# Performance work log

Hardware: AMD Instinct MI355X
Metric: run time of the kernel (lower is better)

The kernel has to match this reference:

```python
import jax, jax.numpy as jnp
import numpy as np

B, L, D, C, N, K = 4096, 4096, 1024, 64, 8192, 5
TEMP = 0.1
ALPHA = 2.0
EPS = 1e-12


def setup_inputs() -> dict:
    key = jax.random.key(0)
    ks = jax.random.split(key, 8)
    x = jax.random.normal(ks[0], (B, 1, L), jnp.float32)
    y = jax.random.randint(ks[1], (B,), 0, C)
    Wf = jax.random.normal(ks[2], (L, D), jnp.float32) * 0.02
    Wc = jax.random.normal(ks[3], (C, D), jnp.float32) * 0.02
    bc = jnp.zeros((C,), jnp.float32)
    supports_old = jax.random.normal(ks[4], (N, D), jnp.float32)
    scores_old = jax.nn.softmax(jax.random.normal(ks[5], (N, C), jnp.float32), axis=-1)
    labels_old = jax.nn.one_hot(jax.random.randint(ks[6], (N,), 0, C), C, dtype=jnp.float32)
    return dict(x=x, y=y, Wf=Wf, Wc=Wc, bc=bc, supports_old=supports_old,
                labels_old=labels_old, scores_old=scores_old)


def _l2n(v, axis):
    return v / jnp.maximum(jnp.linalg.norm(v, axis=axis, keepdims=True), EPS)


def _masked_mean(v, w):
    return jnp.sum(v * w) / jnp.maximum(jnp.sum(w), 1.0)


def _tta_loss(x, Wf, Wc, bc, supports_old, labels_old, scores_old):
    feats = x.reshape(B, L) @ Wf                      # [B, D] featurizer
    logits = feats @ Wc.T + bc                        # [B, C]
    probs = jax.nn.softmax(logits, -1)
    logp = jax.nn.log_softmax(logits, -1)
    prob = probs.max(-1)
    pred = jnp.argmax(logits, -1)
    # prediction-confidence filter
    y_certain = prob >= prob.mean()
    # input-energy entropy filter (scipy.stats.entropy over axis=2)
    px = x * x
    px = px / jnp.maximum(px.sum(2, keepdims=True), EPS)
    e = -(px * jnp.log(px + 1e-30)).sum(2).reshape(B)
    e_certain = e < e.mean()
    w_c = (e_certain & y_certain).astype(jnp.float32)  # certain mask as weights
    w_u = 1.0 - w_c
    yhat = jax.nn.one_hot(pred, C, dtype=jnp.float32)
    # --- memory bank concat + prototype build (no_grad in torch) ---
    sup_all = jnp.concatenate([supports_old, feats], 0)        # [N+B, D]
    lab_all = jnp.concatenate([labels_old, yhat], 0)           # [N+B, C]
    w_all = jnp.concatenate([jnp.ones((N,), jnp.float32), w_c], 0)
    lw = lab_all * w_all[:, None]
    protos = _l2n(sup_all, 1).T @ lw / jnp.maximum(lw.sum(0, keepdims=True), EPS)
    protos = jax.lax.stop_gradient(_l2n(protos, 0))            # [D, C]
    # --- loss1: Tsallis entropy - diversity on balanced probs ---
    m = jnp.sum(probs * w_c[:, None], 0) / jnp.maximum(w_c.sum(), 1.0)
    pb = probs / jnp.maximum(m, EPS)
    pb = pb / pb.sum(1, keepdims=True)
    tsallis = jnp.mean((1.0 - jnp.sum(pb ** ALPHA, 1)) / (ALPHA - 1.0))
    pm = pb.mean(0)
    div = -jnp.sum(pm * jnp.log(pm + EPS))
    loss1 = tsallis - div
    # --- loss2: PCL, prototype CE on certain samples (temp=1) ---
    lp = jax.nn.log_softmax(_l2n(feats, 1) @ protos, -1)       # [B, C]
    ce = -jnp.take_along_axis(lp, pred[:, None], 1)[:, 0]
    loss2 = _masked_mean(ce, w_c)
    # --- loss3: NCL, kNN soft targets from memory bank, uncertain rows ---
    scores_all = jax.lax.stop_gradient(jnp.concatenate([scores_old, probs], 0))
    sup_det = jax.lax.stop_gradient(sup_all)
    sim = _l2n(feats, 1) @ _l2n(sup_det, 1).T / TEMP           # [B, N+B]
    sim = jnp.where(w_all[None, :] > 0, sim, -jnp.inf)
    _, idx = jax.lax.top_k(sim, K)                             # [B, K]
    tgt = scores_all[idx].mean(1)                              # [B, C]
    ncl = -(tgt * logp).sum(1)
    loss3 = _masked_mean(ncl, w_u)
    return loss1 + loss2 + loss3


def reference(x, y, Wf, Wc, bc, supports_old, labels_old, scores_old):
    return _tta_loss(x, Wf, Wc, bc, supports_old, labels_old, scores_old)
```

## Files before the change

kernel.cpp:

```cpp
#include <hip/hip_runtime.h>
#include <math.h>

#define BBATCH 4096
#define LLEN   4096
#define DDIM   1024
#define CCLS   64
#define NSUP   8192
#define NTOT   12288
#define FEPS   1e-12f
#define KCHUNK 48
#define KCAND  (KCHUNK*6)

#define SC_SUMP  0
#define SC_SUME  1
#define SC_SUMWC 2
#define SC_TSAL  3
#define SC_L2NUM 4
#define SC_L3NUM 5

typedef _Float16 half4_t __attribute__((ext_vector_type(4)));
typedef _Float16 half8_t __attribute__((ext_vector_type(8)));
typedef float    f32x4   __attribute__((ext_vector_type(4)));
typedef float    f32x16  __attribute__((ext_vector_type(16)));

static const size_t OFF_FEATS  = 0;
static const size_t OFF_FEATP1 = OFF_FEATS  + (size_t)BBATCH*DDIM;
static const size_t OFF_WFTH   = OFF_FEATP1 + (size_t)BBATCH*DDIM;
static const size_t OFF_WFTL   = OFF_WFTH   + (size_t)DDIM*LLEN/2;
static const size_t OFF_PROBS  = OFF_WFTL   + (size_t)DDIM*LLEN/2;
static const size_t OFF_LOGP   = OFF_PROBS  + (size_t)BBATCH*CCLS;
static const size_t OFF_FNORM  = OFF_LOGP   + (size_t)BBATCH*CCLS;
static const size_t OFF_SNORM  = OFF_FNORM  + BBATCH;
static const size_t OFF_PMAX   = OFF_SNORM  + NSUP;
static const size_t OFF_EROW   = OFF_PMAX   + BBATCH;
static const size_t OFF_WC     = OFF_EROW   + BBATCH;
static const size_t OFF_PRED   = OFF_WC     + BBATCH;
static const size_t OFF_RB     = OFF_PRED   + BBATCH;
static const size_t OFF_SNM    = OFF_RB     + BBATCH;
static const size_t OFF_PROTOT = OFF_SNM    + NTOT;
static const size_t OFF_CVAL   = OFF_PROTOT + (size_t)CCLS*DDIM;
static const size_t OFF_CIDX   = OFF_CVAL   + (size_t)BBATCH*KCAND;
static const size_t OFF_ZERO   = OFF_CIDX   + (size_t)BBATCH*KCAND;
static const size_t OFF_MACC   = OFF_ZERO;
static const size_t OFF_PMACC  = OFF_MACC   + CCLS;
static const size_t OFF_COLS   = OFF_PMACC  + CCLS;
static const size_t OFF_SCAL   = OFF_COLS   + CCLS;
static const size_t OFF_PROTUN = OFF_SCAL   + 32;
static const size_t OFF_ZEND   = OFF_PROTUN + (size_t)DDIM*CCLS;
static const size_t OFF_HT     = OFF_ZEND;
static const size_t WS_END     = OFF_HT + (size_t)32*NTOT*32/2;

__device__ __forceinline__ float waveSum(float v){
  #pragma unroll
  for (int o = 32; o > 0; o >>= 1) v += __shfl_xor(v, o);
  return v;
}
__device__ __forceinline__ float waveMax(float v){
  #pragma unroll
  for (int o = 32; o > 0; o >>= 1) v = fmaxf(v, __shfl_xor(v, o));
  return v;
}
__device__ __forceinline__ float blockSum256(float v, float* sh4){
  v = waveSum(v);
  if ((threadIdx.x & 63) == 0) sh4[threadIdx.x >> 6] = v;
  __syncthreads();
  float r = sh4[0] + sh4[1] + sh4[2] + sh4[3];
  __syncthreads();
  return r;
}
__device__ __forceinline__ void top6_insert(float* v, int* ix, float s, int si){
  bool c0=s>v[0],c1=s>v[1],c2=s>v[2],c3=s>v[3],c4=s>v[4],c5=s>v[5];
  v[5]=c5?(c4?v[4]:s):v[5]; ix[5]=c5?(c4?ix[4]:si):ix[5];
  v[4]=c4?(c3?v[3]:s):v[4]; ix[4]=c4?(c3?ix[3]:si):ix[4];
  v[3]=c3?(c2?v[2]:s):v[3]; ix[3]=c3?(c2?ix[2]:si):ix[3];
  v[2]=c2?(c1?v[1]:s):v[2]; ix[2]=c2?(c1?ix[1]:si):ix[2];
  v[1]=c1?(c0?v[0]:s):v[1]; ix[1]=c1?(c0?ix[0]:si):ix[1];
  v[0]=c0?s:v[0];           ix[0]=c0?si:ix[0];
}
__device__ __forceinline__ void split4(const float4 v, half4_t* h, half4_t* l){
  half4_t hh, ll;
  hh[0] = (_Float16)v.x; hh[1] = (_Float16)v.y; hh[2] = (_Float16)v.z; hh[3] = (_Float16)v.w;
  ll[0] = (_Float16)(v.x - (float)hh[0]);
  ll[1] = (_Float16)(v.y - (float)hh[1]);
  ll[2] = (_Float16)(v.z - (float)hh[2]);
  ll[3] = (_Float16)(v.w - (float)hh[3]);
  *h = hh; *l = ll;
}
__device__ __forceinline__ void split8(const float4 a, const float4 b,
                                       half8_t* h, half8_t* l){
  half8_t hh, ll;
  hh[0]=(_Float16)a.x; hh[1]=(_Float16)a.y; hh[2]=(_Float16)a.z; hh[3]=(_Float16)a.w;
  hh[4]=(_Float16)b.x; hh[5]=(_Float16)b.y; hh[6]=(_Float16)b.z; hh[7]=(_Float16)b.w;
  ll[0]=(_Float16)(a.x-(float)hh[0]); ll[1]=(_Float16)(a.y-(float)hh[1]);
  ll[2]=(_Float16)(a.z-(float)hh[2]); ll[3]=(_Float16)(a.w-(float)hh[3]);
  ll[4]=(_Float16)(b.x-(float)hh[4]); ll[5]=(_Float16)(b.y-(float)hh[5]);
  ll[6]=(_Float16)(b.z-(float)hh[6]); ll[7]=(_Float16)(b.w-(float)hh[7]);
  *h = hh; *l = ll;
}
__device__ __forceinline__ size_t ht_off(int row, int d){
  int kt = d >> 5;
  int slot = ((d >> 3) & 3) ^ ((row >> 3) & 3);
  return (size_t)kt * (NTOT*32) + (size_t)row * 32 + slot*8 + (d & 7);
}

__global__ __launch_bounds__(256)
void k_entropy(const float* __restrict__ x, float* __restrict__ e_row,
               float* __restrict__ scal){
  __shared__ __align__(16) float lx[LLEN];
  __shared__ float sh4[4];
  int row = blockIdx.x, t = threadIdx.x;
  const float4* xr = (const float4*)(x + (size_t)row * LLEN);
  float s = 0.f;
  #pragma unroll
  for (int i = 0; i < 4; ++i){
    float4 v = xr[t + 256*i];
    ((float4*)lx)[t + 256*i] = v;
    s += v.x*v.x + v.y*v.y + v.z*v.z + v.w*v.w;
  }
  s = blockSum256(s, sh4);
  float inv = 1.0f / fmaxf(s, FEPS);
  float ent = 0.f;
  #pragma unroll
  for (int i = 0; i < 4; ++i){
    float4 v = ((float4*)lx)[t + 256*i];
    float p;
    p = v.x*v.x*inv; ent -= p * logf(p + 1e-30f);
    p = v.y*v.y*inv; ent -= p * logf(p + 1e-30f);
    p = v.z*v.z*inv; ent -= p * logf(p + 1e-30f);
    p = v.w*v.w*inv; ent -= p * logf(p + 1e-30f);
  }
  ent = blockSum256(ent, sh4);
  if (t == 0){ e_row[row] = ent; atomicAdd(&scal[SC_SUME], ent); }
}

__global__ __launch_bounds__(256)
void k_wft(const float* __restrict__ Wf, unsigned short* __restrict__ WftH,
           unsigned short* __restrict__ WftL){
  __shared__ __align__(16) float ld[64*68];
  int t = threadIdx.x;
  int d0 = blockIdx.x * 64;
  int l0 = blockIdx.y * 64;
  #pragma unroll
  for (int i = 0; i < 4; ++i){
    int flat = t + 256*i;
    int l = flat >> 4, d4 = (flat & 15) * 4;
    *(float4*)&ld[l*68 + d4] = *(const float4*)(Wf + (size_t)(l0+l)*DDIM + d0 + d4);
  }
  __syncthreads();
  #pragma unroll
  for (int i = 0; i < 4; ++i){
    int flat = t + 256*i;
    int d = flat >> 4, l4 = (flat & 15) * 4;
    float4 v = make_float4(ld[(l4+0)*68 + d], ld[(l4+1)*68 + d],
                           ld[(l4+2)*68 + d], ld[(l4+3)*68 + d]);
    half4_t h, l;
    split4(v, &h, &l);
    *(half4_t*)(WftH + (size_t)(d0+d)*LLEN + l0 + l4) = h;
    *(half4_t*)(WftL + (size_t)(d0+d)*LLEN + l0 + l4) = l;
  }
}

#define SUBH 4096

__global__ __launch_bounds__(256)
void k_feats_mfma(const float* __restrict__ X, const unsigned short* __restrict__ WftHu,
                  const unsigned short* __restrict__ WftLu, float* __restrict__ featp){
  __shared__ __align__(16) _Float16 lds[2*4*SUBH];
  int t = threadIdx.x;
  int n0 = blockIdx.x * 128;
  int m0 = blockIdx.y * 128;
  int kz = blockIdx.z;
  int w = t >> 6, lane = t & 63;
  int wr = w >> 1, wc = w & 1;
  int l31 = lane & 31, hi = lane >> 5;
  const _Float16* Bgh = (const _Float16*)WftHu + (size_t)n0*LLEN;
  const _Float16* Bgl = (const _Float16*)WftLu + (size_t)n0*LLEN;
  const size_t glRow = (size_t)(lane >> 2)*LLEN;
  int ra = t >> 1;
  int kg8 = (t & 1) * 16;
  int aswz = (ra >> 3) & 3;
  const float* Ag = X + (size_t)(m0 + ra)*LLEN + kg8;
  f32x16 acc[2][2];
  #pragma unroll
  for (int i=0;i<2;++i){
    #pragma unroll
    for (int j=0;j<2;++j) acc[i][j] = (f32x16)(0.f);
  }
  const int kstart = kz*2048;

  #define STAGE_B(bufi, k0c) do {                                                 \
    _Float16* Lb = lds + (bufi)*(4*SUBH);                                         \
    _Pragma("unroll")                                                             \
    for (int s2 = 0; s2 < 2; ++s2){                                               \
      int blk = s2*4 + w;                                                         \
      int csrc = (lane & 3) ^ ((blk*2 + (lane >> 5)) & 3);                        \
      size_t go = glRow + (size_t)blk*16*LLEN + (k0c) + (size_t)csrc*8;           \
      __builtin_amdgcn_global_load_lds(                                           \
        (const __attribute__((address_space(1))) void*)(Bgh + go),                \
        (__attribute__((address_space(3))) void*)(Lb + 2*SUBH + blk*512), 16,0,0);\
      __builtin_amdgcn_global_load_lds(                                           \
        (const __attribute__((address_space(1))) void*)(Bgl + go),                \
        (__attribute__((address_space(3))) void*)(Lb + 3*SUBH + blk*512), 16,0,0);\
    }                                                                             \
  } while(0)

  STAGE_B(0, kstart);
  float4 avs[4];
  #pragma unroll
  for (int i=0;i<4;++i) avs[i] = *(const float4*)(Ag + kstart + 4*i);
  int cur = 0;
  int swz = (l31 >> 3) & 3;
  for (int it = 0; it < 64; ++it){
    _Float16* Ah = lds + cur*(4*SUBH);
    _Float16* Al = Ah + SUBH;
    #pragma unroll
    for (int c2 = 0; c2 < 2; ++c2){
      half8_t hv, lv;
      split8(avs[2*c2], avs[2*c2+1], &hv, &lv);
      int slot = ((kg8 >> 3) + c2) ^ aswz;
      *(half8_t*)&Ah[ra*32 + slot*8] = hv;
      *(half8_t*)&Al[ra*32 + slot*8] = lv;
    }
    __syncthreads();
    if (it < 63){
      int kn = kstart + (it+1)*32;
      STAGE_B(cur ^ 1, kn);
      #pragma unroll
      for (int i=0;i<4;++i) avs[i] = *(const float4*)(Ag + kn + 4*i);
      __builtin_amdgcn_sched_barrier(0);
    }
    const _Float16* Bh = lds + cur*(4*SUBH) + 2*SUBH;
    const _Float16* Bl = Bh + SUBH;
    #pragma unroll
    for (int kf = 0; kf < 2; ++kf){
      int sc = (kf*2 + hi) ^ swz;
      half8_t ahf[2], alf[2], bhf[2], blf[2];
      #pragma unroll
      for (int mi=0;mi<2;++mi){
        int off = (wr*64 + mi*32 + l31)*32 + sc*8;
        ahf[mi] = *(const half8_t*)&Ah[off];
        alf[mi] = *(const half8_t*)&Al[off];
      }
      #pragma unroll
      for (int ni=0;ni<2;++ni){
        int off = (wc*64 + ni*32 + l31)*32 + sc*8;
        bhf[ni] = *(const half8_t*)&Bh[off];
        blf[ni] = *(const half8_t*)&Bl[off];
      }
      #pragma unroll
      for (int mi=0;mi<2;++mi){
        #pragma unroll
        for (int ni=0;ni<2;++ni){
          acc[mi][ni] = __builtin_amdgcn_mfma_f32_32x32x16_f16(ahf[mi], bhf[ni], acc[mi][ni], 0,0,0);
          acc[mi][ni] = __builtin_amdgcn_mfma_f32_32x32x16_f16(ahf[mi], blf[ni], acc[mi][ni], 0,0,0);
          acc[mi][ni] = __builtin_amdgcn_mfma_f32_32x32x16_f16(alf[mi], bhf[ni], acc[mi][ni], 0,0,0);
        }
      }
    }
    cur ^= 1;
  }
  #undef STAGE_B
  float* outp = featp + (size_t)kz * BBATCH * DDIM;
  #pragma unroll
  for (int mi=0;mi<2;++mi){
    #pragma unroll
    for (int ni=0;ni<2;++ni){
      #pragma unroll
      for (int r=0;r<16;++r){
        int row = m0 + wr*64 + mi*32 + (r&3) + 8*(r>>2) + 4*hi;
        int col = n0 + wc*64 + ni*32 + l31;
        outp[(size_t)row*DDIM + col] = acc[mi][ni][r];
      }
    }
  }
}

__global__ __launch_bounds__(256)
void k_supnorm(const float* __restrict__ sup, float* __restrict__ snorm,
               _Float16* __restrict__ ht){
  int w = threadIdx.x >> 6, lane = threadIdx.x & 63;
  int row = blockIdx.x*4 + w;
  const float4* rp = (const float4*)(sup + (size_t)row * DDIM);
  float s = 0.f;
  #pragma unroll
  for (int j=0;j<4;++j){
    float4 v = rp[lane + 64*j];
    half4_t h;
    h[0]=(_Float16)v.x; h[1]=(_Float16)v.y; h[2]=(_Float16)v.z; h[3]=(_Float16)v.w;
    int d = (lane + 64*j)*4;
    *(half4_t*)(ht + ht_off(row, d)) = h;
    s += v.x*v.x+v.y*v.y+v.z*v.z+v.w*v.w;
  }
  s = waveSum(s);
  if (lane==0) snorm[row] = sqrtf(s);
}

__global__ __launch_bounds__(256)
void k_logits(float* __restrict__ feats, const float* __restrict__ featp1,
              const float* __restrict__ Wc,
              const float* __restrict__ bc, float* __restrict__ probs,
              float* __restrict__ logp, float* __restrict__ pmax,
              int* __restrict__ pred, float* __restrict__ fnorm,
              float* __restrict__ scal,
              _Float16* __restrict__ ht){
  __shared__ __align__(16) float f[DDIM];
  __shared__ float z[CCLS];
  __shared__ float sh4[4];
  int row = blockIdx.x, t = threadIdx.x;
  const float4* fr0 = (const float4*)(feats  + (size_t)row * DDIM);
  const float4* fr1 = (const float4*)(featp1 + (size_t)row * DDIM);
  float ss = 0.f;
  { float4 a = fr0[t], b = fr1[t];
    float4 v = make_float4(a.x+b.x, a.y+b.y, a.z+b.z, a.w+b.w);
    ((float4*)f)[t] = v;
    ((float4*)(feats + (size_t)row*DDIM))[t] = v;
    half4_t h;
    h[0]=(_Float16)v.x; h[1]=(_Float16)v.y; h[2]=(_Float16)v.z; h[3]=(_Float16)v.w;
    *(half4_t*)(ht + ht_off(NSUP + row, t*4)) = h;
    ss += v.x*v.x+v.y*v.y+v.z*v.z+v.w*v.w; }
  ss = blockSum256(ss, sh4);
  if (t==0) fnorm[row] = sqrtf(ss);
  int w = t >> 6, lane = t & 63;
  for (int ci = 0; ci < 16; ++ci){
    int c = w*16 + ci;
    const float4* wc = (const float4*)(Wc + (size_t)c * DDIM);
    float d = 0.f;
    #pragma unroll
    for (int j=0;j<4;++j){
      float4 a = wc[lane + 64*j];
      float4 b = ((float4*)f)[lane + 64*j];
      d += a.x*b.x+a.y*b.y+a.z*b.z+a.w*b.w;
    }
    d = waveSum(d);
    if (lane == 0) z[c] = d + bc[c];
  }
  __syncthreads();
  if (w == 0){
    float zz = z[lane];
    float m = waveMax(zz);
    unsigned long long bal = __ballot(zz == m);
    int am = __ffsll(bal) - 1;
    float ex = expf(zz - m);
    float sv = waveSum(ex);
    probs[(size_t)row*CCLS + lane] = ex / sv;
    logp[(size_t)row*CCLS + lane]  = (zz - m) - logf(sv);
    if (lane == 0){
      float pmv = 1.0f / sv;
      pmax[row] = pmv;
      pred[row] = am;
      atomicAdd(&scal[SC_SUMP], pmv);
    }
  }
}

__global__ __launch_bounds__(256)
void k_mask(const float* __restrict__ e_row, const float* __restrict__ pmax,
            const float* __restrict__ fnorm, const float* __restrict__ snorm,
            const int* __restrict__ pred, float* __restrict__ w_c,
            float* __restrict__ rb, float* __restrict__ snm,
            float* __restrict__ colsum, float* __restrict__ scal){
  int i = blockIdx.x * 256 + threadIdx.x;
  if (i < NSUP) snm[i] = 1.0f / fmaxf(snorm[i], FEPS);
  if (i < BBATCH){
    float me = scal[SC_SUME] * (1.0f/BBATCH);
    float mp = scal[SC_SUMP] * (1.0f/BBATCH);
    float wc = ((e_row[i] < me) && (pmax[i] >= mp)) ? 1.0f : 0.0f;
    w_c[i] = wc;
    float fn = fmaxf(fnorm[i], FEPS);
    rb[i] = 10.0f / fn;
    snm[NSUP + i] = (wc > 0.f) ? (1.0f / fn) : -1.0f;
    atomicAdd(&scal[SC_SUMWC], wc);
    atomicAdd(&colsum[pred[i]], wc);
  }
}

__global__ __launch_bounds__(256)
void k_colsum_labels(const float* __restrict__ labels, float* __restrict__ colsum){
  int t = threadIdx.x, c = t & 63, sub = t >> 6;
  int r0 = blockIdx.x * 256;
  float s = 0.f;
  for (int i = 0; i < 64; ++i){
    int r = r0 + sub + 4*i;
    s += labels[(size_t)r*CCLS + c];
  }
  __shared__ float loc[4][64];
  loc[sub][c] = s;
  __syncthreads();
  if (sub == 0) atomicAdd(&colsum[c], loc[0][c]+loc[1][c]+loc[2][c]+loc[3][c]);
}

__global__ __launch_bounds__(256)
void k_m_accum(const float* __restrict__ probs, const float* __restrict__ w_c,
               float* __restrict__ m_acc){
  int t = threadIdx.x, c = t & 63, sub = t >> 6;
  int r0 = blockIdx.x * 64;
  float s = 0.f;
  for (int i = 0; i < 16; ++i){
    int r = r0 + sub + 4*i;
    s += probs[(size_t)r*CCLS + c] * w_c[r];
  }
  __shared__ float loc[4][64];
  loc[sub][c] = s;
  __syncthreads();
  if (sub == 0) atomicAdd(&m_acc[c], loc[0][c]+loc[1][c]+loc[2][c]+loc[3][c]);
}

__global__ __launch_bounds__(256)
void k_loss1(const float* __restrict__ probs, const float* __restrict__ m_acc,
             float* __restrict__ pm_acc, float* __restrict__ scal){
  int t = threadIdx.x, w = t >> 6, lane = t & 63;
  float swc = fmaxf(scal[SC_SUMWC], 1.0f);
  float minv = 1.0f / fmaxf(m_acc[lane] / swc, FEPS);
  float pml = 0.f, tsl = 0.f;
  int r0 = blockIdx.x * 64 + w * 16;
  for (int i = 0; i < 16; ++i){
    int r = r0 + i;
    float pb = probs[(size_t)r*CCLS + lane] * minv;
    float t1 = waveSum(pb);
    float t2 = waveSum(pb*pb);
    tsl += 1.0f - t2/(t1*t1);
    pml += pb/t1;
  }
  atomicAdd(&pm_acc[lane], pml);
  if (lane == 0) atomicAdd(&scal[SC_TSAL], tsl);
}

__global__ __launch_bounds__(256)
void k_protos_gemm(const float* __restrict__ sup, const float* __restrict__ feats,
                   const float* __restrict__ labels, const int* __restrict__ pred,
                   const float* __restrict__ w_c, const float* __restrict__ snm,
                   float* __restrict__ protos_un){
  __shared__ __align__(16) float ssx[64*68];
  __shared__ __align__(16) float sl[64*68];
  int t = threadIdx.x;
  int d0 = blockIdx.x * 64;
  int nbase = blockIdx.y * 1536;
  int dg = t & 15, cg = t >> 4;
  float acc[4][4];
  #pragma unroll
  for (int i=0;i<4;++i){
    #pragma unroll
    for (int j=0;j<4;++j) acc[i][j]=0.f;
  }
  for (int n0 = 0; n0 < 1536; n0 += 64){
    __syncthreads();
    #pragma unroll
    for (int i = 0; i < 4; ++i){
      int fidx = t + 256*i;
      int r = fidx >> 4;
      int dc = (fidx & 15) * 4;
      int n = nbase + n0 + r;
      const float* rp = (n < NSUP) ? (sup + (size_t)n*DDIM)
                                   : (feats + (size_t)(n-NSUP)*DDIM);
      *(float4*)&ssx[r*68 + dc] = *(const float4*)(rp + d0 + dc);
    }
    #pragma unroll
    for (int i = 0; i < 4; ++i){
      int fidx = t + 256*i;
      int r = fidx >> 4;
      int cc = (fidx & 15) * 4;
      int n = nbase + n0 + r;
      float sc = snm[n];
      float4 v;
      if (n < NSUP){
        float4 lb = *(const float4*)(labels + (size_t)n*CCLS + cc);
        v.x = lb.x*sc; v.y = lb.y*sc; v.z = lb.z*sc; v.w = lb.w*sc;
      } else {
        int b = n - NSUP;
        float base = w_c[b] * sc;
        int p = pred[b];
        v.x = (p == cc+0) ? base : 0.f;
        v.y = (p == cc+1) ? base : 0.f;
        v.z = (p == cc+2) ? base : 0.f;
        v.w = (p == cc+3) ? base : 0.f;
      }
      *(float4*)&sl[r*68 + cc] = v;
    }
    __syncthreads();
    #pragma unroll 4
    for (int kk = 0; kk < 64; ++kk){
      float4 a = *(float4*)&ssx[kk*68 + 4*dg];
      float4 b = *(float4*)&sl[kk*68 + 4*cg];
      float av[4] = {a.x,a.y,a.z,a.w};
      float bv[4] = {b.x,b.y,b.z,b.w};
      #pragma unroll
      for (int i=0;i<4;++i){
        #pragma unroll
        for (int j=0;j<4;++j) acc[i][j] = fmaf(av[i], bv[j], acc[i][j]);
      }
    }
  }
  #pragma unroll
  for (int i=0;i<4;++i){
    #pragma unroll
    for (int j=0;j<4;++j)
      atomicAdd(&protos_un[(size_t)(d0 + 4*dg + i)*CCLS + 4*cg + j], acc[i][j]);
  }
}

__global__ __launch_bounds__(256)
void k_protos_norm(const float* __restrict__ protos_un, const float* __restrict__ colsum,
                   float* __restrict__ protos_t){
  int c = blockIdx.x, t = threadIdx.x;
  __shared__ float sh4[4];
  float cs = fmaxf(colsum[c], FEPS);
  float v[4];
  float ss = 0.f;
  #pragma unroll
  for (int i=0;i<4;++i){
    int d = t + 256*i;
    v[i] = protos_un[(size_t)d*CCLS + c] / cs;
    ss += v[i]*v[i];
  }
  ss = blockSum256(ss, sh4);
  float inv = 1.0f / fmaxf(sqrtf(ss), FEPS);
  #pragma unroll
  for (int i=0;i<4;++i){
    int d = t + 256*i;
    protos_t[(size_t)c*DDIM + d] = v[i]*inv;
  }
}

__global__ __launch_bounds__(256)
void k_loss2(const float* __restrict__ feats, const float* __restrict__ protos_t,
             const int* __restrict__ pred, const float* __restrict__ w_c,
             const float* __restrict__ fnorm, float* __restrict__ scal){
  int row = blockIdx.x, t = threadIdx.x;
  float wc = w_c[row];
  if (wc == 0.f) return;
  __shared__ __align__(16) float f[DDIM];
  __shared__ float z[CCLS];
  float inv = 1.0f / fmaxf(fnorm[row], FEPS);
  { float4 v = ((const float4*)(feats + (size_t)row*DDIM))[t];
    v.x*=inv; v.y*=inv; v.z*=inv; v.w*=inv;
    ((float4*)f)[t] = v; }
  __syncthreads();
  int w = t >> 6, lane = t & 63;
  for (int ci=0; ci<16; ++ci){
    int c = w*16+ci;
    const float4* pc = (const float4*)(protos_t + (size_t)c*DDIM);
    float d = 0.f;
    #pragma unroll
    for (int j=0;j<4;++j){
      float4 a = pc[lane + 64*j];
      float4 b = ((float4*)f)[lane + 64*j];
      d += a.x*b.x+a.y*b.y+a.z*b.z+a.w*b.w;
    }
    d = waveSum(d);
    if (lane==0) z[c] = d;
  }
  __syncthreads();
  if (w == 0){
    float zz = z[lane];
    float m = waveMax(zz);
    float sv = waveSum(expf(zz - m));
    if (lane == 0){
      float lse = m + logf(sv);
      float ce = lse - z[pred[row]];
      atomicAdd(&scal[SC_L2NUM], ce * wc);
    }
  }
}

__global__ __launch_bounds__(1024, 1)
void k_sim_approx(const _Float16* __restrict__ ht, const float* __restrict__ snm,
                  float* __restrict__ cval, int* __restrict__ cidx){
  __shared__ __align__(16) _Float16 lds[2*16384];
  __shared__ float sns[256];
  int t = threadIdx.x;
  int w = t >> 6, lane = t & 63;
  int wr = w >> 2, wcn = w & 3;
  int l31 = lane & 31, hi = lane >> 5;
  int bidl = blockIdx.y * 48 + blockIdx.x;
  int xcd = bidl & 7, lin = bidl >> 3;
  int yb = xcd * 2 + (lin / 48);
  int xb = lin - (lin / 48) * 48;
  int m0 = xb * 256, n0 = yb * 256;
  if (t < 256) sns[t] = snm[m0 + t];
  const _Float16* Abase = ht + (size_t)(m0 + w*16)*32 + (size_t)lane*8;
  const _Float16* Bbase = ht + (size_t)(NSUP + n0 + w*16)*32 + (size_t)lane*8;
  f32x16 acc[2][2];
  #pragma unroll
  for (int i=0;i<2;++i){
    #pragma unroll
    for (int j=0;j<2;++j) acc[i][j] = (f32x16)(0.f);
  }

  #define SIM_ST(b, kt) do {                                                      \
    __builtin_amdgcn_global_load_lds(                                             \
      (const __attribute__((address_space(1))) void*)(Abase + (size_t)(kt)*(NTOT*32)),\
      (__attribute__((address_space(3))) void*)(lds + (b)*16384 + w*512), 16,0,0);\
    __builtin_amdgcn_global_load_lds(                                             \
      (const __attribute__((address_space(1))) void*)(Bbase + (size_t)(kt)*(NTOT*32)),\
      (__attribute__((address_space(3))) void*)(lds + (b)*16384 + 8192 + w*512), 16,0,0);\
  } while(0)

  SIM_ST(0, 0);
  for (int kt = 0; kt < 32; ++kt){
    const _Float16* buf = lds + (kt&1)*16384;
    __syncthreads();
    half8_t af[2][2], bf[2][2];
    #pragma unroll
    for (int p=0;p<2;++p){
      int Ra = wr*64 + p*32 + l31;
      int sw = (Ra>>3)&3;
      #pragma unroll
      for (int kf=0;kf<2;++kf)
        af[p][kf] = *(const half8_t*)(buf + Ra*32 + (((kf*2+hi)^sw))*8);
    }
    #pragma unroll
    for (int ni=0;ni<2;++ni){
      int Rb = wcn*64 + ni*32 + l31;
      int sw = (Rb>>3)&3;
      #pragma unroll
      for (int kf=0;kf<2;++kf)
        bf[ni][kf] = *(const half8_t*)(buf + 8192 + Rb*32 + (((kf*2+hi)^sw))*8);
    }
    if (kt < 31) SIM_ST((kt+1)&1, kt+1);
    __builtin_amdgcn_s_setprio(1);
    #pragma unroll
    for (int p=0;p<2;++p){
      #pragma unroll
      for (int ni=0;ni<2;++ni){
        #pragma unroll
        for (int kf=0;kf<2;++kf)
          acc[p][ni] = __builtin_amdgcn_mfma_f32_32x32x16_f16(af[p][kf], bf[ni][kf], acc[p][ni], 0,0,0);
      }
    }
    __builtin_amdgcn_s_setprio(0);
  }
  #undef SIM_ST
  __syncthreads();
  float tv[2][6]; int ti[2][6];
  #pragma unroll
  for (int ni=0;ni<2;++ni){
    #pragma unroll
    for (int k=0;k<6;++k){ tv[ni][k] = -INFINITY; ti[ni][k] = 0x7fffffff; }
  }
  #pragma unroll
  for (int ni=0;ni<2;++ni){
    #pragma unroll
    for (int p=0;p<2;++p){
      #pragma unroll
      for (int r=0;r<16;++r){
        int rl = wr*64 + p*32 + (r&3) + 8*(r>>2) + 4*hi;
        float sn = sns[rl];
        float v = acc[p][ni][r] * fabsf(sn);
        v = (sn > 0.f) ? v : -INFINITY;
        top6_insert(tv[ni], ti[ni], v, m0 + rl);
      }
    }
  }
  #pragma unroll
  for (int ni=0;ni<2;++ni){
    float pv[6]; int pi[6];
    #pragma unroll
    for (int k=0;k<6;++k){ pv[k] = __shfl_xor(tv[ni][k], 32); pi[k] = __shfl_xor(ti[ni][k], 32); }
    #pragma unroll
    for (int k=0;k<6;++k) top6_insert(tv[ni], ti[ni], pv[k], pi[k]);
  }
  float* MV = (float*)lds;
  int*   MI = (int*)lds + 6400;
  if (hi == 0){
    #pragma unroll
    for (int ni=0;ni<2;++ni){
      int col = wcn*64 + ni*32 + l31;
      #pragma unroll
      for (int k=0;k<6;++k){
        MV[col*25 + wr*6 + k] = tv[ni][k];
        MI[col*25 + wr*6 + k] = ti[ni][k];
      }
    }
  }
  __syncthreads();
  if (t < 256){
    float bv[6]; int bi[6];
    #pragma unroll
    for (int k=0;k<6;++k){ bv[k] = -INFINITY; bi[k] = 0x7fffffff; }
    for (int j = 0; j < 24; ++j) top6_insert(bv, bi, MV[t*25 + j], MI[t*25 + j]);
    float* co = cval + (size_t)(n0 + t)*KCAND + xb*6;
    int*   ci = cidx + (size_t)(n0 + t)*KCAND + xb*6;
    #pragma unroll
    for (int k=0;k<6;++k){ co[k] = bv[k]; ci[k] = bi[k]; }
  }
}

__global__ __launch_bounds__(256)
void k_rescore_ncl(const float* __restrict__ cval, const int* __restrict__ cidx,
                   const float* __restrict__ sup, const float* __restrict__ feats,
                   const float* __restrict__ rb, const float* __restrict__ snm,
                   const float* __restrict__ scores_old, const float* __restrict__ probs,
                   const float* __restrict__ logp, const float* __restrict__ w_c,
                   float* __restrict__ scal){
  int t = threadIdx.x, w = t >> 6, lane = t & 63;
  int b = blockIdx.x*4 + w;
  float lv[5]; int li[5];
  #pragma unroll
  for (int j=0;j<5;++j){
    int idx = lane + 64*j;
    bool ok = idx < KCAND;
    lv[j] = ok ? cval[(size_t)b*KCAND + idx] : -INFINITY;
    li[j] = ok ? cidx[(size_t)b*KCAND + idx] : 0x7fffffff;
  }
  #pragma unroll
  for (int a=0;a<4;++a){
    #pragma unroll
    for (int c=0;c<4-a;++c){
      bool sw = lv[c+1] > lv[c];
      float fv = sw ? lv[c+1] : lv[c];  float fw = sw ? lv[c] : lv[c+1];
      int   iv = sw ? li[c+1] : li[c];  int   iw = sw ? li[c] : li[c+1];
      lv[c]=fv; lv[c+1]=fw; li[c]=iv; li[c+1]=iw;
    }
  }
  float t10v[10]; int t10i[10];
  int head = 0;
  #pragma unroll
  for (int k=0;k<10;++k){
    float hv = -INFINITY; int hidx = 0x7fffffff;
    switch(head){
      case 0: hv=lv[0]; hidx=li[0]; break;
      case 1: hv=lv[1]; hidx=li[1]; break;
      case 2: hv=lv[2]; hidx=li[2]; break;
      case 3: hv=lv[3]; hidx=li[3]; break;
      case 4: hv=lv[4]; hidx=li[4]; break;
      default: break;
    }
    float m = waveMax(hv);
    unsigned long long bal = __ballot(hv == m);
    int wl = __ffsll(bal) - 1;
    t10v[k] = m;
    t10i[k] = __shfl(hidx, wl);
    if (lane == wl) head++;
  }
  (void)t10v;
  float4 fr0 = *(const float4*)(feats + (size_t)b*DDIM + lane*16);
  float4 fr1 = *(const float4*)(feats + (size_t)b*DDIM + lane*16 + 4);
  float4 fr2 = *(const float4*)(feats + (size_t)b*DDIM + lane*16 + 8);
  float4 fr3 = *(const float4*)(feats + (size_t)b*DDIM + lane*16 + 12);
  float rbv = rb[b];
  float ev[10];
  #pragma unroll
  for (int c=0;c<10;++c){
    int idx = t10i[c];
    const float* srow = (idx < NSUP) ? (sup + (size_t)idx*DDIM)
                                     : (feats + (size_t)(idx-NSUP)*DDIM);
    float4 s0 = *(const float4*)(srow + lane*16);
    float4 s1 = *(const float4*)(srow + lane*16 + 4);
    float4 s2 = *(const float4*)(srow + lane*16 + 8);
    float4 s3 = *(const float4*)(srow + lane*16 + 12);
    float d = fr0.x*s0.x + fr0.y*s0.y + fr0.z*s0.z + fr0.w*s0.w
            + fr1.x*s1.x + fr1.y*s1.y + fr1.z*s1.z + fr1.w*s1.w
            + fr2.x*s2.x + fr2.y*s2.y + fr2.z*s2.z + fr2.w*s2.w
            + fr3.x*s3.x + fr3.y*s3.y + fr3.z*s3.z + fr3.w*s3.w;
    d = waveSum(d);
    ev[c] = d * rbv * fabsf(snm[idx]);
  }
  int used = 0;
  int sel[5];
  #pragma unroll
  for (int k=0;k<5;++k){
    float bb = -INFINITY; int bbi = 0x7fffffff; int bj = 0;
    #pragma unroll
    for (int j=0;j<10;++j){
      bool free_ = !((used >> j) & 1);
      bool better = free_ && ((ev[j] > bb) || (ev[j] == bb && t10i[j] < bbi));
      bb  = better ? ev[j]   : bb;
      bbi = better ? t10i[j] : bbi;
      bj  = better ? j       : bj;
    }
    used |= (1 << bj);
    sel[k] = bbi;
  }
  float tg = 0.f;
  #pragma unroll
  for (int k=0;k<5;++k){
    int ix = sel[k];
    const float* srow = (ix < NSUP) ? (scores_old + (size_t)ix*CCLS)
                                    : (probs + (size_t)(ix-NSUP)*CCLS);
    tg += srow[lane];
  }
  tg *= 0.2f;
  float d = tg * logp[(size_t)b*CCLS + lane];
  d = waveSum(d);
  if (lane == 0) atomicAdd(&scal[SC_L3NUM], -d * (1.0f - w_c[b]));
}

__global__ void k_final(const float* __restrict__ pm_acc, const float* __restrict__ scal,
                        float* __restrict__ out){
  int lane = threadIdx.x;
  float pm = pm_acc[lane] * (1.0f/BBATCH);
  float dterm = pm * logf(pm + FEPS);
  float dv = waveSum(dterm);
  if (lane == 0){
    float div = -dv;
    float tsallis = scal[SC_TSAL] * (1.0f/BBATCH);
    float swc = scal[SC_SUMWC];
    float l1 = tsallis - div;
    float l2 = scal[SC_L2NUM] / fmaxf(swc, 1.0f);
    float l3 = scal[SC_L3NUM] / fmaxf((float)BBATCH - swc, 1.0f);
    out[0] = l1 + l2 + l3;
  }
}

extern "C" void kernel_launch(void* const* d_in, const int* in_sizes, int n_in,
                              void* d_out, int out_size, void* d_ws, size_t ws_size,
                              hipStream_t stream){
  (void)in_sizes; (void)n_in; (void)out_size; (void)ws_size;
  const float* x      = (const float*)d_in[0];
  const float* Wf     = (const float*)d_in[2];
  const float* Wc     = (const float*)d_in[3];
  const float* bc     = (const float*)d_in[4];
  const float* sup    = (const float*)d_in[5];
  const float* labels = (const float*)d_in[6];
  const float* scores = (const float*)d_in[7];
  float* ws = (float*)d_ws;

  float* feats  = ws + OFF_FEATS;
  float* featp1 = ws + OFF_FEATP1;
  unsigned short* wfth = (unsigned short*)(ws + OFF_WFTH);
  unsigned short* wftl = (unsigned short*)(ws + OFF_WFTL);
  _Float16* ht  = (_Float16*)(ws + OFF_HT);
  float* probs  = ws + OFF_PROBS;
  float* logp   = ws + OFF_LOGP;
  float* fnorm  = ws + OFF_FNORM;
  float* snorm  = ws + OFF_SNORM;
  float* pmax   = ws + OFF_PMAX;
  float* e_row  = ws + OFF_EROW;
  float* w_c    = ws + OFF_WC;
  int*   pred   = (int*)(ws + OFF_PRED);
  float* rb     = ws + OFF_RB;
  float* snm    = ws + OFF_SNM;
  float* protot = ws + OFF_PROTOT;
  float* cvalp  = ws + OFF_CVAL;
  int*   cidxp  = (int*)(ws + OFF_CIDX);
  float* m_acc  = ws + OFF_MACC;
  float* pm_acc = ws + OFF_PMACC;
  float* colsum = ws + OFF_COLS;
  float* scal   = ws + OFF_SCAL;
  float* protun = ws + OFF_PROTUN;

  hipMemsetAsync(ws + OFF_ZERO, 0, (OFF_ZEND - OFF_ZERO)*sizeof(float), stream);

  k_entropy      <<<BBATCH, 256, 0, stream>>>(x, e_row, scal);
  k_wft          <<<dim3(DDIM/64, LLEN/64), 256, 0, stream>>>(Wf, wfth, wftl);
  k_feats_mfma   <<<dim3(DDIM/128, BBATCH/128, 2), 256, 0, stream>>>(x, wfth, wftl, feats);
  k_supnorm      <<<NSUP/4, 256, 0, stream>>>(sup, snorm, ht);
  k_logits       <<<BBATCH, 256, 0, stream>>>(feats, featp1, Wc, bc, probs, logp, pmax, pred, fnorm, scal, ht);
  k_mask         <<<32, 256, 0, stream>>>(e_row, pmax, fnorm, snorm, pred, w_c, rb, snm, colsum, scal);
  k_colsum_labels<<<32, 256, 0, stream>>>(labels, colsum);
  k_m_accum      <<<64, 256, 0, stream>>>(probs, w_c, m_acc);
  k_loss1        <<<64, 256, 0, stream>>>(probs, m_acc, pm_acc, scal);
  k_protos_gemm  <<<dim3(16, 8), 256, 0, stream>>>(sup, feats, labels, pred, w_c, snm, protun);
  k_protos_norm  <<<CCLS, 256, 0, stream>>>(protun, colsum, protot);
  k_loss2        <<<BBATCH, 256, 0, stream>>>(feats, protot, pred, w_c, fnorm, scal);
  k_sim_approx   <<<dim3(48, 16), 1024, 0, stream>>>(ht, snm, cvalp, cidxp);
  k_rescore_ncl  <<<BBATCH/4, 256, 0, stream>>>(cvalp, cidxp, sup, feats, rb, snm, scores, probs, logp, w_c, scal);
  k_final        <<<1, 64, 0, stream>>>(pm_acc, scal, (float*)d_out);
}
```

Before: 819.7 us.

## Stage fp32 A tiles via direct global-to-LDS loads and split at fragment load

The A operand (x) is now copied straight into LDS as fp32 with global_load_lds, using an XOR swizzle, instead of going through registers, being split to fp16 hi/lo and written to LDS by each thread. The hi/lo split moves to fragment-load time, and all fragments are read before the next stage's async loads are issued. MFMA issue priority is also raised with s_setprio. This is meant to remove the register round trip and VALU work from the staging path and to overlap loads with compute. The cost is that each wave redoes the split per fragment and the A tile takes twice the LDS space in fp32.

```diff
diff --git a/kernel.cpp b/kernel.cpp
--- a/kernel.cpp
+++ b/kernel.cpp
@@ -86,17 +86,6 @@
   ll[3] = (_Float16)(v.w - (float)hh[3]);
   *h = hh; *l = ll;
 }
-__device__ __forceinline__ void split8(const float4 a, const float4 b,
-                                       half8_t* h, half8_t* l){
-  half8_t hh, ll;
-  hh[0]=(_Float16)a.x; hh[1]=(_Float16)a.y; hh[2]=(_Float16)a.z; hh[3]=(_Float16)a.w;
-  hh[4]=(_Float16)b.x; hh[5]=(_Float16)b.y; hh[6]=(_Float16)b.z; hh[7]=(_Float16)b.w;
-  ll[0]=(_Float16)(a.x-(float)hh[0]); ll[1]=(_Float16)(a.y-(float)hh[1]);
-  ll[2]=(_Float16)(a.z-(float)hh[2]); ll[3]=(_Float16)(a.w-(float)hh[3]);
-  ll[4]=(_Float16)(b.x-(float)hh[4]); ll[5]=(_Float16)(b.y-(float)hh[5]);
-  ll[6]=(_Float16)(b.z-(float)hh[6]); ll[7]=(_Float16)(b.w-(float)hh[7]);
-  *h = hh; *l = ll;
-}
 __device__ __forceinline__ size_t ht_off(int row, int d){
   int kt = d >> 5;
   int slot = ((d >> 3) & 3) ^ ((row >> 3) & 3);
@@ -160,12 +149,10 @@
   }
 }
 
-#define SUBH 4096
-
 __global__ __launch_bounds__(256)
 void k_feats_mfma(const float* __restrict__ X, const unsigned short* __restrict__ WftHu,
                   const unsigned short* __restrict__ WftLu, float* __restrict__ featp){
-  __shared__ __align__(16) _Float16 lds[2*4*SUBH];
+  __shared__ __align__(16) _Float16 lds[2*16384];
   int t = threadIdx.x;
   int n0 = blockIdx.x * 128;
   int m0 = blockIdx.y * 128;
@@ -175,11 +162,9 @@
   int l31 = lane & 31, hi = lane >> 5;
   const _Float16* Bgh = (const _Float16*)WftHu + (size_t)n0*LLEN;
   const _Float16* Bgl = (const _Float16*)WftLu + (size_t)n0*LLEN;
-  const size_t glRow = (size_t)(lane >> 2)*LLEN;
-  int ra = t >> 1;
-  int kg8 = (t & 1) * 16;
-  int aswz = (ra >> 3) & 3;
-  const float* Ag = X + (size_t)(m0 + ra)*LLEN + kg8;
+  const size_t glRowB = (size_t)(lane >> 2)*LLEN;
+  int arow = lane >> 3;
+  int agr  = (lane & 7) ^ (arow & 7);
   f32x16 acc[2][2];
   #pragma unroll
   for (int i=0;i<2;++i){
@@ -188,78 +173,82 @@
   }
   const int kstart = kz*2048;
 
-  #define STAGE_B(bufi, k0c) do {                                                 \
-    _Float16* Lb = lds + (bufi)*(4*SUBH);                                         \
-    _Pragma("unroll")                                                             \
-    for (int s2 = 0; s2 < 2; ++s2){                                               \
-      int blk = s2*4 + w;                                                         \
-      int csrc = (lane & 3) ^ ((blk*2 + (lane >> 5)) & 3);                        \
-      size_t go = glRow + (size_t)blk*16*LLEN + (k0c) + (size_t)csrc*8;           \
-      __builtin_amdgcn_global_load_lds(                                           \
-        (const __attribute__((address_space(1))) void*)(Bgh + go),                \
-        (__attribute__((address_space(3))) void*)(Lb + 2*SUBH + blk*512), 16,0,0);\
-      __builtin_amdgcn_global_load_lds(                                           \
-        (const __attribute__((address_space(1))) void*)(Bgl + go),                \
-        (__attribute__((address_space(3))) void*)(Lb + 3*SUBH + blk*512), 16,0,0);\
-    }                                                                             \
+  #define STAGE_AB(bufi, k0c) do {                                                 \
+    _Float16* Lb = lds + (bufi)*16384;                                             \
+    _Pragma("unroll")                                                              \
+    for (int g = 0; g < 4; ++g){                                                   \
+      const float* asrc = X + (size_t)(m0 + w*32 + g*8 + arow)*LLEN + (k0c) + 4*agr;\
+      __builtin_amdgcn_global_load_lds(                                            \
+        (const __attribute__((address_space(1))) void*)asrc,                       \
+        (__attribute__((address_space(3))) void*)(Lb + (w*32 + g*8)*64), 16,0,0);  \
+    }                                                                              \
+    _Pragma("unroll")                                                              \
+    for (int s2 = 0; s2 < 2; ++s2){                                                \
+      int blk = s2*4 + w;                                                          \
+      int csrc = (lane & 3) ^ ((blk*2 + (lane >> 5)) & 3);                         \
+      size_t go = glRowB + (size_t)blk*16*LLEN + (k0c) + (size_t)csrc*8;           \
+      __builtin_amdgcn_global_load_lds(                                            \
+        (const __attribute__((address_space(1))) void*)(Bgh + go),                 \
+        (__attribute__((address_space(3))) void*)(Lb + 8192 + blk*512), 16,0,0);   \
+      __builtin_amdgcn_global_load_lds(                                            \
+        (const __attribute__((address_space(1))) void*)(Bgl + go),                 \
+        (__attribute__((address_space(3))) void*)(Lb + 12288 + blk*512), 16,0,0);  \
+    }                                                                              \
   } while(0)
 
-  STAGE_B(0, kstart);
-  float4 avs[4];
-  #pragma unroll
-  for (int i=0;i<4;++i) avs[i] = *(const float4*)(Ag + kstart + 4*i);
-  int cur = 0;
-  int swz = (l31 >> 3) & 3;
+  STAGE_AB(0, kstart);
   for (int it = 0; it < 64; ++it){
-    _Float16* Ah = lds + cur*(4*SUBH);
-    _Float16* Al = Ah + SUBH;
-    #pragma unroll
-    for (int c2 = 0; c2 < 2; ++c2){
-      half8_t hv, lv;
-      split8(avs[2*c2], avs[2*c2+1], &hv, &lv);
-      int slot = ((kg8 >> 3) + c2) ^ aswz;
-      *(half8_t*)&Ah[ra*32 + slot*8] = hv;
-      *(half8_t*)&Al[ra*32 + slot*8] = lv;
-    }
+    const _Float16* buf = lds + (it&1)*16384;
     __syncthreads();
-    if (it < 63){
-      int kn = kstart + (it+1)*32;
-      STAGE_B(cur ^ 1, kn);
-      #pragma unroll
-      for (int i=0;i<4;++i) avs[i] = *(const float4*)(Ag + kn + 4*i);
-      __builtin_amdgcn_sched_barrier(0);
-    }
-    const _Float16* Bh = lds + cur*(4*SUBH) + 2*SUBH;
-    const _Float16* Bl = Bh + SUBH;
-    #pragma unroll
-    for (int kf = 0; kf < 2; ++kf){
-      int sc = (kf*2 + hi) ^ swz;
-      half8_t ahf[2], alf[2], bhf[2], blf[2];
-      #pragma unroll
-      for (int mi=0;mi<2;++mi){
-        int off = (wr*64 + mi*32 + l31)*32 + sc*8;
-        ahf[mi] = *(const half8_t*)&Ah[off];
-        alf[mi] = *(const half8_t*)&Al[off];
+    const float* Af = (const float*)buf;
+    half8_t ah[2][2], al[2][2];
+    #pragma unroll
+    for (int p_=0;p_<2;++p_){
+      int Ra = wr*64 + p_*32 + l31;
+      int rx = Ra & 7;
+      #pragma unroll
+      for (int kf=0;kf<2;++kf){
+        int g0 = kf*4 + hi*2;
+        f32x4 v0 = *(const f32x4*)(Af + Ra*32 + 4*((g0  ) ^ rx));
+        f32x4 v1 = *(const f32x4*)(Af + Ra*32 + 4*((g0+1) ^ rx));
+        half8_t h, l;
+        #pragma unroll
+        for (int j=0;j<4;++j){
+          h[j]   = (_Float16)v0[j]; l[j]   = (_Float16)(v0[j] - (float)h[j]);
+          h[4+j] = (_Float16)v1[j]; l[4+j] = (_Float16)(v1[j] - (float)h[4+j]);
+        }
+        ah[p_][kf] = h; al[p_][kf] = l;
       }
+    }
+    half8_t bh[2][2], bl[2][2];
+    #pragma unroll
+    for (int ni=0;ni<2;++ni){
+      int Rb = wc*64 + ni*32 + l31;
+      int sw = (Rb>>3)&3;
+      #pragma unroll
+      for (int kf=0;kf<2;++kf){
+        int sc = (kf*2 + hi) ^ sw;
+        bh[ni][kf] = *(const half8_t*)(buf + 8192  + Rb*32 + sc*8);
+        bl[ni][kf] = *(const half8_t*)(buf + 12288 + Rb*32 + sc*8);
+      }
+    }
+    if (it < 63) STAGE_AB((it+1)&1, kstart + (it+1)*32);
+    __builtin_amdgcn_s_setprio(1);
+    #pragma unroll
+    for (int p_=0;p_<2;++p_){
       #pragma unroll
       for (int ni=0;ni<2;++ni){
-        int off = (wc*64 + ni*32 + l31)*32 + sc*8;
-        bhf[ni] = *(const half8_t*)&Bh[off];
-        blf[ni] = *(const half8_t*)&Bl[off];
-      }
-      #pragma unroll
-      for (int mi=0;mi<2;++mi){
         #pragma unroll
-        for (int ni=0;ni<2;++ni){
-          acc[mi][ni] = __builtin_amdgcn_mfma_f32_32x32x16_f16(ahf[mi], bhf[ni], acc[mi][ni], 0,0,0);
-          acc[mi][ni] = __builtin_amdgcn_mfma_f32_32x32x16_f16(ahf[mi], blf[ni], acc[mi][ni], 0,0,0);
-          acc[mi][ni] = __builtin_amdgcn_mfma_f32_32x32x16_f16(alf[mi], bhf[ni], acc[mi][ni], 0,0,0);
+        for (int kf=0;kf<2;++kf){
+          acc[p_][ni] = __builtin_amdgcn_mfma_f32_32x32x16_f16(ah[p_][kf], bh[ni][kf], acc[p_][ni], 0,0,0);
+          acc[p_][ni] = __builtin_amdgcn_mfma_f32_32x32x16_f16(ah[p_][kf], bl[ni][kf], acc[p_][ni], 0,0,0);
+          acc[p_][ni] = __builtin_amdgcn_mfma_f32_32x32x16_f16(al[p_][kf], bh[ni][kf], acc[p_][ni], 0,0,0);
         }
       }
     }
-    cur ^= 1;
-  }
-  #undef STAGE_B
+    __builtin_amdgcn_s_setprio(0);
+  }
+  #undef STAGE_AB
   float* outp = featp + (size_t)kz * BBATCH * DDIM;
   #pragma unroll
   for (int mi=0;mi<2;++mi){
```

Result: no change. 822.1 us (+0.3%).
